# Optimization experiments

Hardware: AMD Instinct MI355X
Metric: run time of the kernel (lower is better)

The kernel has to match this reference:

```python
import jax, jax.numpy as jnp
import numpy as np

S, D = 16384, 1024


def setup_inputs() -> dict:
    key = jax.random.key(0)
    ks = jax.random.split(key, 7)
    stdv = 1.0 / np.sqrt(D)
    u = lambda k, shape: jax.random.uniform(k, shape, jnp.float32, -stdv, stdv)
    return {
        "x": jax.random.normal(ks[0], (S, D), jnp.float32),
        "Wq": u(ks[1], (D, D)), "bq": u(ks[2], (D,)),
        "Wk": u(ks[3], (D, D)), "bk": u(ks[4], (D,)),
        "Wv": u(ks[5], (D, D)), "bv": u(ks[6], (D,)),
    }


def reference(x, Wq, bq, Wk, bk, Wv, bv):
    # torch.nn.Linear: y = x @ W^T + b
    q = x @ Wq.T + bq          # [S, D]
    k = x @ Wk.T + bk          # [S, D]
    v = x @ Wv.T + bv          # [S, D]
    d = x.shape[-1]
    # NOTE: faithful to source -- scores are over the FEATURE axis: [D, D]
    scores = jnp.einsum('sd,se->de', q, k) / jnp.sqrt(jnp.float32(d))
    attn = jax.nn.softmax(scores, axis=-1)   # [D, D]
    out = v @ attn                           # [S, D]
    return out, attn
```

## Files before the change

kernel.cpp:

```cpp
#include <hip/hip_runtime.h>
#include <hip/hip_bf16.h>
#include <stdint.h>


#define S_ 16384
#define D_ 1024

typedef _Float16 half8 __attribute__((ext_vector_type(8)));
typedef _Float16 half4 __attribute__((ext_vector_type(4)));
typedef float f32x4 __attribute__((ext_vector_type(4)));

__device__ __forceinline__ void gload_lds16(const _Float16* g, _Float16* l) {
    __builtin_amdgcn_global_load_lds(
        (const __attribute__((address_space(1))) void*)g,
        (__attribute__((address_space(3))) void*)l, 16, 0, 0);
}

#define VM8() do { asm volatile("s_waitcnt vmcnt(8)" ::: "memory"); __builtin_amdgcn_sched_barrier(0); } while (0)
#define VM0() do { asm volatile("s_waitcnt vmcnt(0)" ::: "memory"); __builtin_amdgcn_sched_barrier(0); } while (0)
#define BAR() __builtin_amdgcn_s_barrier()
#define LGKM0() do { asm volatile("s_waitcnt lgkmcnt(0)" ::: "memory"); __builtin_amdgcn_sched_barrier(0); } while (0)
#define LGKM8() do { asm volatile("s_waitcnt lgkmcnt(8)" ::: "memory"); __builtin_amdgcn_sched_barrier(0); } while (0)
#define PRIO1() __builtin_amdgcn_s_setprio(1)
#define PRIO0() __builtin_amdgcn_s_setprio(0)

#define STAGEA(H, KT, NX) do { \
    const _Float16* _s = srcA + (size_t)((H) * 128) * lda + (size_t)(KT) * 64; \
    _Float16* _d = AsS + (NX) * 16384 + ((H) * 128 + 8 * w) * 64; \
    gload_lds16(_s, _d); \
    gload_lds16(_s + (size_t)64 * lda, _d + 4096); \
} while (0)

#define STAGEB(H, KT, NX) do { \
    const _Float16* _s = srcB + (size_t)((H) * 128) * ldb + (size_t)(KT) * 64; \
    _Float16* _d = BsS + (NX) * 16384 + ((H) * 128 + 8 * w) * 64; \
    gload_lds16(_s, _d); \
    gload_lds16(_s + (size_t)64 * ldb, _d + 4096); \
} while (0)

#define READA(PA, QA) do { _Pragma("unroll") \
    for (int fm = 0; fm < 4; ++fm) { \
        af[fm][0] = *(const half8*)((PA) + (((QA) * 128 + fm * 16) << 7) + cx0); \
        af[fm][1] = *(const half8*)((PA) + (((QA) * 128 + fm * 16) << 7) + cx1); } \
} while (0)

#define READB(PB, BF, QB) do { _Pragma("unroll") \
    for (int fn = 0; fn < 2; ++fn) { \
        BF[fn][0] = *(const half8*)((PB) + (((QB) * 128 + fn * 16) << 7) + cx0); \
        BF[fn][1] = *(const half8*)((PB) + (((QB) * 128 + fn * 16) << 7) + cx1); } \
} while (0)

#define MFMAB(QA, QB, BF) do { _Pragma("unroll") \
    for (int fm = 0; fm < 4; ++fm) { _Pragma("unroll") \
        for (int fn = 0; fn < 2; ++fn) { \
            f32x4 _c = acc[(QA) * 4 + fm][(QB) * 2 + fn]; \
            _c = __builtin_amdgcn_mfma_f32_16x16x32_f16(af[fm][0], BF[fn][0], _c, 0, 0, 0); \
            _c = __builtin_amdgcn_mfma_f32_16x16x32_f16(af[fm][1], BF[fn][1], _c, 0, 0, 0); \
            acc[(QA) * 4 + fm][(QB) * 2 + fn] = _c; } } \
} while (0)

template <int F16OUT, int BIAS>
__global__ __launch_bounds__(512, 2)
void gemm256(const _Float16* __restrict__ A, const _Float16* __restrict__ B,
             void* __restrict__ C, const float* __restrict__ bias,
             int lda, int ldb, int ldc, int ksub, long long mn,
             int ntx, int ntxy, int cpx) {
    __shared__ _Float16 As[2][16384];
    __shared__ _Float16 Bs[2][16384];
    const int t = threadIdx.x;
    const int l = t & 63;
    const int w = t >> 6;
    const int wm = w >> 2, wn = w & 3;

    const int hb = blockIdx.x;
    const int lg = (hb & 7) * cpx + (hb >> 3);
    const int bz = lg / ntxy;
    const int rem = lg - bz * ntxy;
    const int by = rem / ntx;
    const int bx = rem - by * ntx;
    const size_t m0 = (size_t)by * 256;
    const size_t n0 = (size_t)bx * 256;
    const size_t k0 = (size_t)bz * (size_t)ksub;
    const long long coff = (long long)bz * mn;

    const int colsw = 8 * ((l & 7) ^ (l >> 3));
    const _Float16* srcA = A + (m0 + 8 * w + (l >> 3)) * (size_t)lda + k0 + colsw;
    const _Float16* srcB = B + (n0 + 8 * w + (l >> 3)) * (size_t)ldb + k0 + colsw;
    _Float16* AsS = &As[0][0];
    _Float16* BsS = &Bs[0][0];

    const int cx0 = (((l >> 4) << 4)) ^ ((l & 7) << 4);
    const int cx1 = (64 + ((l >> 4) << 4)) ^ ((l & 7) << 4);
    const char* basePA = (const char*)AsS + ((wm * 64 + (l & 15)) << 7);
    const char* basePB = (const char*)BsS + ((wn * 32 + (l & 15)) << 7);

    f32x4 acc[8][4] = {};
    half8 af[4][2], bf0[2][2], bf1[2][2];

    const int nk = ksub >> 6;

    STAGEA(0, 0, 0); STAGEB(0, 0, 0); STAGEB(1, 0, 0); STAGEA(1, 0, 0);
    STAGEA(0, 1, 1); STAGEB(0, 1, 1); STAGEB(1, 1, 1); STAGEA(1, 1, 1);

    for (int kt = 0; kt < nk; ++kt) {
        const int p = kt & 1;
        const int ks = kt + 2;
        const bool hs = ks < nk;
        const char* pA = basePA + p * 32768;
        const char* pB = basePB + p * 32768;

        if (kt == nk - 1) VM0(); else VM8();
        BAR();

        READA(pA, 0); READB(pB, bf0, 0);
        LGKM8();
        BAR(); LGKM0();
        PRIO1(); MFMAB(0, 0, bf0); PRIO0(); BAR();

        READB(pB, bf1, 1);
        if (hs) { STAGEA(0, ks, p); STAGEB(0, ks, p); }
        BAR(); LGKM0();
        PRIO1(); MFMAB(0, 1, bf1); PRIO0(); BAR();

        READA(pA, 1);
        if (hs) STAGEB(1, ks, p);
        BAR(); LGKM0();
        PRIO1(); MFMAB(1, 1, bf1); PRIO0(); BAR();

        if (hs) STAGEA(1, ks, p);
        PRIO1(); MFMAB(1, 0, bf0); PRIO0(); BAR();
    }

    char* lmy = (char*)AsS + w * 16384;
    const int cr = (l >> 4) << 2;
    const int cc = l & 15;

    if (F16OUT) {
        _Float16* lw = (_Float16*)lmy;
#pragma unroll
        for (int h = 0; h < 2; ++h) {
#pragma unroll
            for (int mm = 0; mm < 4; ++mm) {
#pragma unroll
                for (int n = 0; n < 4; ++n) {
                    const int lcol = (n >> 1) * 32 + (n & 1) * 16 + cc;
                    const int lrow = mm * 16 + cr;
#pragma unroll
                    for (int r = 0; r < 4; ++r)
                        lw[(lrow + r) * 68 + lcol] = (_Float16)acc[4 * h + mm][n][r];
                }
            }
            LGKM0();
            const size_t grow0 = m0 + (size_t)h * 128 + wm * 64;
#pragma unroll
            for (int i = 0; i < 32; ++i) {
                const int lrow = i * 2 + (l >> 5);
                const int lcol2 = (l & 31) * 2;
                const uint32_t v = *(const uint32_t*)(lw + lrow * 68 + lcol2);
                const int qb = lcol2 >> 5;
                const size_t col = n0 + qb * 128 + wn * 32 + (lcol2 & 31);
                *(uint32_t*)((_Float16*)C + coff + (long long)(grow0 + lrow) * ldc + col) = v;
            }
            LGKM0();
        }
    } else {
        float* lw = (float*)lmy;
        float bb4[4];
#pragma unroll
        for (int n = 0; n < 4; ++n) {
            const size_t col = n0 + (n >> 1) * 128 + wn * 32 + (n & 1) * 16 + cc;
            bb4[n] = BIAS ? bias[col] : 0.f;
        }
#pragma unroll
        for (int h = 0; h < 4; ++h) {
#pragma unroll
            for (int mm = 0; mm < 2; ++mm) {
#pragma unroll
                for (int n = 0; n < 4; ++n) {
                    const int lcol = (n >> 1) * 32 + (n & 1) * 16 + cc;
                    const int lrow = mm * 16 + cr;
#pragma unroll
                    for (int r = 0; r < 4; ++r)
                        lw[(lrow + r) * 68 + lcol] = acc[2 * h + mm][n][r] + bb4[n];
                }
            }
            LGKM0();
            const size_t grow0 = m0 + (size_t)(h >> 1) * 128 + wm * 64 + (h & 1) * 32;
#pragma unroll
            for (int i = 0; i < 8; ++i) {
                const int lrow = i * 4 + (l >> 4);
                const int lcol = (l & 15) * 4;
                const f32x4 v = *(const f32x4*)(lw + lrow * 68 + lcol);
                const int qb = lcol >> 5;
                const size_t col = n0 + qb * 128 + wn * 32 + (lcol & 31);
                *(f32x4*)((float*)C + coff + (long long)(grow0 + lrow) * ldc + col) = v;
            }
            LGKM0();
        }
    }
}

__global__ __launch_bounds__(256, 2)
void gemm_abt(const _Float16* __restrict__ A, const _Float16* __restrict__ B,
              float* __restrict__ C, const float* __restrict__ bias,
              int bias_mode, int lda, int ldb, int ldc, int ksub,
              float scale, long long mn) {
    const int t = threadIdx.x;
    const int lane = t & 63;
    const int wave = t >> 6;
    const int wr = (wave >> 1) * 64;
    const int wc = (wave & 1) * 64;
    const size_t m0 = (size_t)blockIdx.y * 128;
    const size_t n0 = (size_t)blockIdx.x * 128;
    const size_t k0 = (size_t)blockIdx.z * (size_t)ksub;
    const long long coff = (long long)blockIdx.z * mn;

    __shared__ _Float16 As[128 * 32];
    __shared__ _Float16 Bs[128 * 32];

    f32x4 acc[4][4] = {};

    const _Float16* a0 = A + (m0 + (size_t)(t >> 2)) * (size_t)lda + k0 + (t & 3) * 8;
    const _Float16* a1 = a0 + (size_t)64 * lda;
    const _Float16* b0 = B + (n0 + (size_t)(t >> 2)) * (size_t)ldb + k0 + (t & 3) * 8;
    const _Float16* b1 = b0 + (size_t)64 * ldb;
    _Float16* AsW0 = As + wave * 512;
    _Float16* AsW1 = As + 2048 + wave * 512;
    _Float16* BsW0 = Bs + wave * 512;
    _Float16* BsW1 = Bs + 2048 + wave * 512;

    const int nk = ksub >> 5;
    for (int kt = 0; kt < nk; ++kt) {
        __syncthreads();
        gload_lds16(a0, AsW0);
        gload_lds16(a1, AsW1);
        gload_lds16(b0, BsW0);
        gload_lds16(b1, BsW1);
        a0 += 32; a1 += 32; b0 += 32; b1 += 32;
        __syncthreads();

        half8 af[4], bf[4];
#pragma unroll
        for (int i = 0; i < 4; ++i)
            af[i] = *(const half8*)(As + (wr + i * 16 + (lane & 15)) * 32 + (lane >> 4) * 8);
#pragma unroll
        for (int i = 0; i < 4; ++i)
            bf[i] = *(const half8*)(Bs + (wc + i * 16 + (lane & 15)) * 32 + (lane >> 4) * 8);
#pragma unroll
        for (int i = 0; i < 4; ++i)
#pragma unroll
            for (int j = 0; j < 4; ++j)
                acc[i][j] = __builtin_amdgcn_mfma_f32_16x16x32_f16(af[i], bf[j], acc[i][j], 0, 0, 0);
    }

    const int cr = (lane >> 4) * 4;
    const int cc = lane & 15;
#pragma unroll
    for (int i = 0; i < 4; ++i) {
#pragma unroll
        for (int j = 0; j < 4; ++j) {
            const size_t row0 = m0 + wr + i * 16 + cr;
            const size_t col = n0 + wc + j * 16 + cc;
            const float bcol = (bias_mode == 2) ? bias[col] : 0.f;
#pragma unroll
            for (int r = 0; r < 4; ++r) {
                float val = acc[i][j][r] * scale + bcol;
                C[coff + (long long)(row0 + r) * ldc + col] = val;
            }
        }
    }
}

__global__ void cast2_f32_f16(const float* __restrict__ inA, _Float16* __restrict__ outA,
                              const float* __restrict__ inB, _Float16* __restrict__ outB,
                              int n8) {
    int i = blockIdx.x * 256 + threadIdx.x;
    const float* in = inA;
    _Float16* out = outA;
    if (i >= n8) { i -= n8; in = inB; out = outB; }
    const f32x4* p = (const f32x4*)in + (size_t)i * 2;
    f32x4 x0 = p[0], x1 = p[1];
    half8 h;
    h[0] = (_Float16)x0[0]; h[1] = (_Float16)x0[1];
    h[2] = (_Float16)x0[2]; h[3] = (_Float16)x0[3];
    h[4] = (_Float16)x1[0]; h[5] = (_Float16)x1[1];
    h[6] = (_Float16)x1[2]; h[7] = (_Float16)x1[3];
    ((half8*)out)[i] = h;
}

template <int WRITE_ROW, int COLSUM>
__global__ __launch_bounds__(256)
void cast_transpose(const float* __restrict__ in, _Float16* __restrict__ outRow,
                    _Float16* __restrict__ outT, float* __restrict__ msum, int ldT) {
    __shared__ _Float16 tile[64][66];
    __shared__ float red[16][16][4];
    const int t = threadIdx.x;
    const int c0 = blockIdx.x * 64;
    const int r0 = blockIdx.y * 64;
    const int cg = t & 15;
    const int rb = t >> 4;
    f32x4 csum = {};
#pragma unroll
    for (int it = 0; it < 4; ++it) {
        const int rr = rb + it * 16;
        f32x4 v = *(const f32x4*)(in + (size_t)(r0 + rr) * 1024 + c0 + cg * 4);
        if (COLSUM) { csum[0] += v[0]; csum[1] += v[1]; csum[2] += v[2]; csum[3] += v[3]; }
        _Float16 h0 = (_Float16)v[0], h1 = (_Float16)v[1];
        _Float16 h2 = (_Float16)v[2], h3 = (_Float16)v[3];
        tile[rr][cg * 4 + 0] = h0; tile[rr][cg * 4 + 1] = h1;
        tile[rr][cg * 4 + 2] = h2; tile[rr][cg * 4 + 3] = h3;
        if (WRITE_ROW) {
            half4 h = {h0, h1, h2, h3};
            *(half4*)(outRow + (size_t)(r0 + rr) * 1024 + c0 + cg * 4) = h;
        }
    }
    if (COLSUM) {
        red[rb][cg][0] = csum[0]; red[rb][cg][1] = csum[1];
        red[rb][cg][2] = csum[2]; red[rb][cg][3] = csum[3];
    }
    __syncthreads();
    if (COLSUM && t < 64) {
        float s = 0.f;
#pragma unroll
        for (int k = 0; k < 16; ++k) s += red[k][t >> 2][t & 3];
        atomicAdd(msum + c0 + t, s);
    }
    const int i = t >> 2, ch = (t & 3) * 16;
    half8 h0v, h1v;
#pragma unroll
    for (int j = 0; j < 8; ++j) h0v[j] = tile[ch + j][i];
#pragma unroll
    for (int j = 0; j < 8; ++j) h1v[j] = tile[ch + 8 + j][i];
    *(half8*)(outT + (size_t)(c0 + i) * ldT + r0 + ch) = h0v;
    *(half8*)(outT + (size_t)(c0 + i) * ldT + r0 + ch + 8) = h1v;
}

__global__ void zero_vec(float* __restrict__ p, int n) {
    int i = blockIdx.x * 256 + threadIdx.x;
    if (i < n) p[i] = 0.f;
}

__global__ __launch_bounds__(256)
void u2w_kernel(const float* __restrict__ Wq, const float* __restrict__ Wk,
                const float* __restrict__ bq, const float* __restrict__ m,
                float* __restrict__ u2, float* __restrict__ w) {
    const int bid = blockIdx.x;
    const int t = threadIdx.x;
    const float* W = (bid < 1024) ? Wq : Wk;
    const int row = (bid < 1024) ? bid : bid - 1024;
    float s = 0.f;
#pragma unroll
    for (int it = 0; it < 4; ++it) {
        const int i = t + it * 256;
        s += W[(size_t)row * 1024 + i] * m[i];
    }
    for (int o = 32; o; o >>= 1) s += __shfl_xor(s, o);
    __shared__ float red[4];
    if ((t & 63) == 0) red[t >> 6] = s;
    __syncthreads();
    if (t == 0) {
        float tot = red[0] + red[1] + red[2] + red[3];
        if (bid < 1024) u2[bid] = tot + 16384.0f * bq[bid];
        else w[row] = tot;
    }
}

__global__ __launch_bounds__(256)
void reduce_g(const _Float16* __restrict__ part, _Float16* __restrict__ G16) {
    const size_t off = ((size_t)blockIdx.x * 256 + threadIdx.x) * 8;
    float s[8] = {};
    for (int z = 0; z < 16; ++z) {
        half8 v = *(const half8*)(part + (size_t)z * 1048576 + off);
#pragma unroll
        for (int j = 0; j < 8; ++j) s[j] += (float)v[j];
    }
    half8 o;
#pragma unroll
    for (int j = 0; j < 8; ++j) o[j] = (_Float16)s[j];
    *(half8*)(G16 + off) = o;
}

__global__ __launch_bounds__(256)
void reduce_cast(const float* __restrict__ part, _Float16* __restrict__ outh,
                 int nz, float scale) {
    const int idx = (blockIdx.x * 256 + threadIdx.x) * 4;
    f32x4 s = {};
    for (int z = 0; z < nz; ++z) {
        f32x4 v = *(const f32x4*)(part + (size_t)z * 1048576 + idx);
        s[0] += v[0]; s[1] += v[1]; s[2] += v[2]; s[3] += v[3];
    }
    half4 h;
    h[0] = (_Float16)(s[0] * scale); h[1] = (_Float16)(s[1] * scale);
    h[2] = (_Float16)(s[2] * scale); h[3] = (_Float16)(s[3] * scale);
    *(half4*)(outh + idx) = h;
}

__global__ __launch_bounds__(256)
void softmax_rows(const float* __restrict__ part, const float* __restrict__ u2,
                  const float* __restrict__ bq, const float* __restrict__ bk,
                  const float* __restrict__ w,
                  float* __restrict__ P, _Float16* __restrict__ PT) {
    const int a = blockIdx.x;
    const int t = threadIdx.x;
    __shared__ float red[8];
    const size_t off = (size_t)a * 1024 + t * 4;
    f32x4 s = {};
#pragma unroll
    for (int z = 0; z < 4; ++z) {
        f32x4 v = *(const f32x4*)(part + (size_t)z * 1048576 + off);
        s[0] += v[0]; s[1] += v[1]; s[2] += v[2]; s[3] += v[3];
    }
    const float ru = u2[a], rb = bq[a];
    f32x4 bk4 = *(const f32x4*)(bk + t * 4);
    f32x4 w4 = *(const f32x4*)(w + t * 4);
#pragma unroll
    for (int j = 0; j < 4; ++j) s[j] = (s[j] + ru * bk4[j] + rb * w4[j]) * 0.03125f;

    float m = fmaxf(fmaxf(s[0], s[1]), fmaxf(s[2], s[3]));
    for (int o = 32; o; o >>= 1) m = fmaxf(m, __shfl_xor(m, o));
    if ((t & 63) == 0) red[t >> 6] = m;
    __syncthreads();
    m = fmaxf(fmaxf(red[0], red[1]), fmaxf(red[2], red[3]));

    float e0 = expf(s[0] - m), e1 = expf(s[1] - m);
    float e2 = expf(s[2] - m), e3 = expf(s[3] - m);
    float sum = e0 + e1 + e2 + e3;
    for (int o = 32; o; o >>= 1) sum += __shfl_xor(sum, o);
    if ((t & 63) == 0) red[4 + (t >> 6)] = sum;
    __syncthreads();
    sum = red[4] + red[5] + red[6] + red[7];
    const float inv = 1.0f / sum;

    f32x4 o4 = {e0 * inv, e1 * inv, e2 * inv, e3 * inv};
    *(f32x4*)(P + off) = o4;
    const int b = t * 4;
    PT[(size_t)(b + 0) * 1024 + a] = (_Float16)o4[0];
    PT[(size_t)(b + 1) * 1024 + a] = (_Float16)o4[1];
    PT[(size_t)(b + 2) * 1024 + a] = (_Float16)o4[2];
    PT[(size_t)(b + 3) * 1024 + a] = (_Float16)o4[3];
}

__global__ __launch_bounds__(256)
void attn_bv(const float* __restrict__ attn, const float* __restrict__ bv,
             float* __restrict__ c) {
    const int j = blockIdx.x * 256 + threadIdx.x;
    const int a0 = blockIdx.y * 64;
    float s = 0.f;
#pragma unroll 4
    for (int k = 0; k < 64; ++k) {
        const int a = a0 + k;
        s += attn[(size_t)a * 1024 + j] * bv[a];
    }
    atomicAdd(c + j, s);
}

extern "C" void kernel_launch(void* const* d_in, const int* in_sizes, int n_in,
                              void* d_out, int out_size, void* d_ws, size_t ws_size,
                              hipStream_t stream) {
    const float* x  = (const float*)d_in[0];
    const float* Wq = (const float*)d_in[1];
    const float* bq = (const float*)d_in[2];
    const float* Wk = (const float*)d_in[3];
    const float* bk = (const float*)d_in[4];
    const float* Wv = (const float*)d_in[5];
    const float* bv = (const float*)d_in[6];
    float* out  = (float*)d_out;
    float* attn = out + (size_t)S_ * D_;

    char* ws = (char*)d_ws;
    float*    part  = (float*)ws;
    _Float16* partH = (_Float16*)ws;
    _Float16* x16   = (_Float16*)(ws + 33554432);
    _Float16* xT16  = (_Float16*)(ws + 67108864);
    _Float16* wq16  = (_Float16*)(ws + 100663296);
    _Float16* wk16  = (_Float16*)(ws + 102760448);
    _Float16* wvT16 = (_Float16*)(ws + 104857600);
    _Float16* G16   = (_Float16*)(ws + 106954752);
    _Float16* U16   = (_Float16*)(ws + 109051904);
    _Float16* PT    = (_Float16*)(ws + 111149056);
    _Float16* MT16  = (_Float16*)(ws + 113246208);
    float*    mvec  = (float*)(ws + 115343360);
    float*    u2    = mvec + 1024;
    float*    wv    = u2 + 1024;
    float*    cvec  = wv + 1024;

    zero_vec<<<16, 256, 0, stream>>>(mvec, 4096);
    cast_transpose<1, 1><<<dim3(16, 256), 256, 0, stream>>>(x, x16, xT16, mvec, S_);
    cast2_f32_f16<<<1024, 256, 0, stream>>>(Wq, wq16, Wk, wk16, D_ * D_ / 8);
    cast_transpose<0, 0><<<dim3(16, 16), 256, 0, stream>>>(Wv, nullptr, wvT16, nullptr, D_);
    u2w_kernel<<<2048, 256, 0, stream>>>(Wq, Wk, bq, mvec, u2, wv);

    gemm256<1, 0><<<256, 512, 0, stream>>>(xT16, xT16, (void*)partH, nullptr,
                                           16384, 16384, 1024, 1024, 1048576LL,
                                           4, 16, 32);
    reduce_g<<<512, 256, 0, stream>>>(partH, G16);
    gemm_abt<<<dim3(8, 8, 4), 256, 0, stream>>>(wq16, G16, part, nullptr, 0,
                                                1024, 1024, 1024, 256, 1.0f, 1048576);
    reduce_cast<<<1024, 256, 0, stream>>>(part, U16, 4, 1.0f);
    gemm_abt<<<dim3(8, 8, 4), 256, 0, stream>>>(U16, wk16, part, nullptr, 0,
                                                1024, 1024, 1024, 256, 1.0f, 1048576);
    softmax_rows<<<1024, 256, 0, stream>>>(part, u2, bq, bk, wv, attn, PT);
    attn_bv<<<dim3(4, 16), 256, 0, stream>>>(attn, bv, cvec);
    gemm_abt<<<dim3(8, 8, 4), 256, 0, stream>>>(PT, wvT16, part, nullptr, 0,
                                                1024, 1024, 1024, 256, 1.0f, 1048576);
    reduce_cast<<<1024, 256, 0, stream>>>(part, MT16, 4, 1.0f);
    gemm256<0, 1><<<256, 512, 0, stream>>>(x16, MT16, (void*)out, cvec,
                                           1024, 1024, 1024, 1024, 0LL,
                                           4, 256, 32);
}
```

Measured before the change: 192.4 us.

## Drop split-K for small GEMMs, fuse epilogues, merge weight prep kernels

The three 1024^3 GEMMs no longer use 4-way split-K with separate reduce kernels. Each now runs the full K loop on an 8x8 grid and writes fp16 or the bias-corrected, scaled scores directly, so softmax only reads scores. The weight cast, Wv transpose and u2/w dot products are merged into one prep kernel, and the big GEMM epilogue stores become nontemporal. This removes launches and partial-sum memory traffic, but each small GEMM now runs only 64 blocks, which leaves most CUs idle.

```diff
diff --git a/kernel.cpp b/kernel.cpp
--- a/kernel.cpp
+++ b/kernel.cpp
@@ -159,7 +159,8 @@
                 const uint32_t v = *(const uint32_t*)(lw + lrow * 68 + lcol2);
                 const int qb = lcol2 >> 5;
                 const size_t col = n0 + qb * 128 + wn * 32 + (lcol2 & 31);
-                *(uint32_t*)((_Float16*)C + coff + (long long)(grow0 + lrow) * ldc + col) = v;
+                __builtin_nontemporal_store(v,
+                    (uint32_t*)((_Float16*)C + coff + (long long)(grow0 + lrow) * ldc + col));
             }
             LGKM0();
         }
@@ -193,18 +194,21 @@
                 const f32x4 v = *(const f32x4*)(lw + lrow * 68 + lcol);
                 const int qb = lcol >> 5;
                 const size_t col = n0 + qb * 128 + wn * 32 + (lcol & 31);
-                *(f32x4*)((float*)C + coff + (long long)(grow0 + lrow) * ldc + col) = v;
+                __builtin_nontemporal_store(v,
+                    (f32x4*)((float*)C + coff + (long long)(grow0 + lrow) * ldc + col));
             }
             LGKM0();
         }
     }
 }
 
+template <int MODE>
 __global__ __launch_bounds__(256, 2)
-void gemm_abt(const _Float16* __restrict__ A, const _Float16* __restrict__ B,
-              float* __restrict__ C, const float* __restrict__ bias,
-              int bias_mode, int lda, int ldb, int ldc, int ksub,
-              float scale, long long mn) {
+void gemm_s(const _Float16* __restrict__ A, const _Float16* __restrict__ B,
+            void* __restrict__ C,
+            const float* __restrict__ u2v, const float* __restrict__ bqv,
+            const float* __restrict__ bkv, const float* __restrict__ wvv,
+            int lda, int ldb, int ldc) {
     const int t = threadIdx.x;
     const int lane = t & 63;
     const int wave = t >> 6;
@@ -212,25 +216,22 @@
     const int wc = (wave & 1) * 64;
     const size_t m0 = (size_t)blockIdx.y * 128;
     const size_t n0 = (size_t)blockIdx.x * 128;
-    const size_t k0 = (size_t)blockIdx.z * (size_t)ksub;
-    const long long coff = (long long)blockIdx.z * mn;
 
     __shared__ _Float16 As[128 * 32];
     __shared__ _Float16 Bs[128 * 32];
 
     f32x4 acc[4][4] = {};
 
-    const _Float16* a0 = A + (m0 + (size_t)(t >> 2)) * (size_t)lda + k0 + (t & 3) * 8;
+    const _Float16* a0 = A + (m0 + (size_t)(t >> 2)) * (size_t)lda + (t & 3) * 8;
     const _Float16* a1 = a0 + (size_t)64 * lda;
-    const _Float16* b0 = B + (n0 + (size_t)(t >> 2)) * (size_t)ldb + k0 + (t & 3) * 8;
+    const _Float16* b0 = B + (n0 + (size_t)(t >> 2)) * (size_t)ldb + (t & 3) * 8;
     const _Float16* b1 = b0 + (size_t)64 * ldb;
     _Float16* AsW0 = As + wave * 512;
     _Float16* AsW1 = As + 2048 + wave * 512;
     _Float16* BsW0 = Bs + wave * 512;
     _Float16* BsW1 = Bs + 2048 + wave * 512;
 
-    const int nk = ksub >> 5;
-    for (int kt = 0; kt < nk; ++kt) {
+    for (int kt = 0; kt < 32; ++kt) {
         __syncthreads();
         gload_lds16(a0, AsW0);
         gload_lds16(a1, AsW1);
@@ -261,31 +262,18 @@
         for (int j = 0; j < 4; ++j) {
             const size_t row0 = m0 + wr + i * 16 + cr;
             const size_t col = n0 + wc + j * 16 + cc;
-            const float bcol = (bias_mode == 2) ? bias[col] : 0.f;
 #pragma unroll
             for (int r = 0; r < 4; ++r) {
-                float val = acc[i][j][r] * scale + bcol;
-                C[coff + (long long)(row0 + r) * ldc + col] = val;
+                if (MODE == 1) {
+                    ((_Float16*)C)[(row0 + r) * (size_t)ldc + col] = (_Float16)acc[i][j][r];
+                } else {
+                    const float val = (acc[i][j][r] + u2v[row0 + r] * bkv[col]
+                                       + bqv[row0 + r] * wvv[col]) * 0.03125f;
+                    ((float*)C)[(row0 + r) * (size_t)ldc + col] = val;
+                }
             }
         }
     }
-}
-
-__global__ void cast2_f32_f16(const float* __restrict__ inA, _Float16* __restrict__ outA,
-                              const float* __restrict__ inB, _Float16* __restrict__ outB,
-                              int n8) {
-    int i = blockIdx.x * 256 + threadIdx.x;
-    const float* in = inA;
-    _Float16* out = outA;
-    if (i >= n8) { i -= n8; in = inB; out = outB; }
-    const f32x4* p = (const f32x4*)in + (size_t)i * 2;
-    f32x4 x0 = p[0], x1 = p[1];
-    half8 h;
-    h[0] = (_Float16)x0[0]; h[1] = (_Float16)x0[1];
-    h[2] = (_Float16)x0[2]; h[3] = (_Float16)x0[3];
-    h[4] = (_Float16)x1[0]; h[5] = (_Float16)x1[1];
-    h[6] = (_Float16)x1[2]; h[7] = (_Float16)x1[3];
-    ((half8*)out)[i] = h;
 }
 
 template <int WRITE_ROW, int COLSUM>
@@ -335,34 +323,83 @@
     *(half8*)(outT + (size_t)(c0 + i) * ldT + r0 + ch + 8) = h1v;
 }
 
+__global__ __launch_bounds__(256)
+void prep_w(const float* __restrict__ Wq, const float* __restrict__ Wk,
+            const float* __restrict__ Wv, const float* __restrict__ bq,
+            const float* __restrict__ m,
+            _Float16* __restrict__ wq16, _Float16* __restrict__ wk16,
+            _Float16* __restrict__ wvT16,
+            float* __restrict__ u2, float* __restrict__ w) {
+    __shared__ _Float16 tile[64][66];
+    __shared__ float wred[4];
+    const int b = blockIdx.x;
+    const int t = threadIdx.x;
+
+    if (b < 1024) {
+        const bool isQ = b < 512;
+        const int bb = isQ ? b : b - 512;
+        const float* W = isQ ? Wq : Wk;
+        _Float16* o = isQ ? wq16 : wk16;
+        const size_t base = (size_t)bb * 2048 + (size_t)t * 8;
+        const f32x4* p = (const f32x4*)(W + base);
+        f32x4 x0 = p[0], x1 = p[1];
+        half8 h;
+        h[0] = (_Float16)x0[0]; h[1] = (_Float16)x0[1];
+        h[2] = (_Float16)x0[2]; h[3] = (_Float16)x0[3];
+        h[4] = (_Float16)x1[0]; h[5] = (_Float16)x1[1];
+        h[6] = (_Float16)x1[2]; h[7] = (_Float16)x1[3];
+        ((half8*)o)[bb * 256 + t] = h;
+        const int col = (t * 8) & 1023;
+        f32x4 m0 = *(const f32x4*)(m + col);
+        f32x4 m1 = *(const f32x4*)(m + col + 4);
+        float s = x0[0] * m0[0] + x0[1] * m0[1] + x0[2] * m0[2] + x0[3] * m0[3]
+                + x1[0] * m1[0] + x1[1] * m1[1] + x1[2] * m1[2] + x1[3] * m1[3];
+        for (int o2 = 32; o2; o2 >>= 1) s += __shfl_xor(s, o2);
+        if ((t & 63) == 0) wred[t >> 6] = s;
+        __syncthreads();
+        if (t == 0) {
+            const int rA = 2 * bb, rB = 2 * bb + 1;
+            const float vA = wred[0] + wred[1];
+            const float vB = wred[2] + wred[3];
+            if (isQ) {
+                u2[rA] = vA + 16384.0f * bq[rA];
+                u2[rB] = vB + 16384.0f * bq[rB];
+            } else {
+                w[rA] = vA;
+                w[rB] = vB;
+            }
+        }
+        return;
+    }
+
+    const int bb = b - 1024;
+    const int c0 = (bb & 15) * 64;
+    const int r0 = (bb >> 4) * 64;
+    const int cg = t & 15;
+    const int rb = t >> 4;
+#pragma unroll
+    for (int it = 0; it < 4; ++it) {
+        const int rr = rb + it * 16;
+        f32x4 v = *(const f32x4*)(Wv + (size_t)(r0 + rr) * 1024 + c0 + cg * 4);
+        tile[rr][cg * 4 + 0] = (_Float16)v[0];
+        tile[rr][cg * 4 + 1] = (_Float16)v[1];
+        tile[rr][cg * 4 + 2] = (_Float16)v[2];
+        tile[rr][cg * 4 + 3] = (_Float16)v[3];
+    }
+    __syncthreads();
+    const int i = t >> 2, ch = (t & 3) * 16;
+    half8 h0v, h1v;
+#pragma unroll
+    for (int j = 0; j < 8; ++j) h0v[j] = tile[ch + j][i];
+#pragma unroll
+    for (int j = 0; j < 8; ++j) h1v[j] = tile[ch + 8 + j][i];
+    *(half8*)(wvT16 + (size_t)(c0 + i) * 1024 + r0 + ch) = h0v;
+    *(half8*)(wvT16 + (size_t)(c0 + i) * 1024 + r0 + ch + 8) = h1v;
+}
+
 __global__ void zero_vec(float* __restrict__ p, int n) {
     int i = blockIdx.x * 256 + threadIdx.x;
     if (i < n) p[i] = 0.f;
-}
-
-__global__ __launch_bounds__(256)
-void u2w_kernel(const float* __restrict__ Wq, const float* __restrict__ Wk,
-                const float* __restrict__ bq, const float* __restrict__ m,
-                float* __restrict__ u2, float* __restrict__ w) {
-    const int bid = blockIdx.x;
-    const int t = threadIdx.x;
-    const float* W = (bid < 1024) ? Wq : Wk;
-    const int row = (bid < 1024) ? bid : bid - 1024;
-    float s = 0.f;
-#pragma unroll
-    for (int it = 0; it < 4; ++it) {
-        const int i = t + it * 256;
-        s += W[(size_t)row * 1024 + i] * m[i];
-    }
-    for (int o = 32; o; o >>= 1) s += __shfl_xor(s, o);
-    __shared__ float red[4];
-    if ((t & 63) == 0) red[t >> 6] = s;
-    __syncthreads();
-    if (t == 0) {
-        float tot = red[0] + red[1] + red[2] + red[3];
-        if (bid < 1024) u2[bid] = tot + 16384.0f * bq[bid];
-        else w[row] = tot;
-    }
 }
 
 __global__ __launch_bounds__(256)
@@ -381,40 +418,13 @@
 }
 
 __global__ __launch_bounds__(256)
-void reduce_cast(const float* __restrict__ part, _Float16* __restrict__ outh,
-                 int nz, float scale) {
-    const int idx = (blockIdx.x * 256 + threadIdx.x) * 4;
-    f32x4 s = {};
-    for (int z = 0; z < nz; ++z) {
-        f32x4 v = *(const f32x4*)(part + (size_t)z * 1048576 + idx);
-        s[0] += v[0]; s[1] += v[1]; s[2] += v[2]; s[3] += v[3];
-    }
-    half4 h;
-    h[0] = (_Float16)(s[0] * scale); h[1] = (_Float16)(s[1] * scale);
-    h[2] = (_Float16)(s[2] * scale); h[3] = (_Float16)(s[3] * scale);
-    *(half4*)(outh + idx) = h;
-}
-
-__global__ __launch_bounds__(256)
-void softmax_rows(const float* __restrict__ part, const float* __restrict__ u2,
-                  const float* __restrict__ bq, const float* __restrict__ bk,
-                  const float* __restrict__ w,
+void softmax_rows(const float* __restrict__ scores,
                   float* __restrict__ P, _Float16* __restrict__ PT) {
     const int a = blockIdx.x;
     const int t = threadIdx.x;
     __shared__ float red[8];
     const size_t off = (size_t)a * 1024 + t * 4;
-    f32x4 s = {};
-#pragma unroll
-    for (int z = 0; z < 4; ++z) {
-        f32x4 v = *(const f32x4*)(part + (size_t)z * 1048576 + off);
-        s[0] += v[0]; s[1] += v[1]; s[2] += v[2]; s[3] += v[3];
-    }
-    const float ru = u2[a], rb = bq[a];
-    f32x4 bk4 = *(const f32x4*)(bk + t * 4);
-    f32x4 w4 = *(const f32x4*)(w + t * 4);
-#pragma unroll
-    for (int j = 0; j < 4; ++j) s[j] = (s[j] + ru * bk4[j] + rb * w4[j]) * 0.03125f;
+    f32x4 s = *(const f32x4*)(scores + off);
 
     float m = fmaxf(fmaxf(s[0], s[1]), fmaxf(s[2], s[3]));
     for (int o = 32; o; o >>= 1) m = fmaxf(m, __shfl_xor(m, o));
@@ -468,7 +478,7 @@
     float* attn = out + (size_t)S_ * D_;
 
     char* ws = (char*)d_ws;
-    float*    part  = (float*)ws;
+    float*    scores = (float*)ws;
     _Float16* partH = (_Float16*)ws;
     _Float16* x16   = (_Float16*)(ws + 33554432);
     _Float16* xT16  = (_Float16*)(ws + 67108864);
@@ -486,24 +496,24 @@
 
     zero_vec<<<16, 256, 0, stream>>>(mvec, 4096);
     cast_transpose<1, 1><<<dim3(16, 256), 256, 0, stream>>>(x, x16, xT16, mvec, S_);
-    cast2_f32_f16<<<1024, 256, 0, stream>>>(Wq, wq16, Wk, wk16, D_ * D_ / 8);
-    cast_transpose<0, 0><<<dim3(16, 16), 256, 0, stream>>>(Wv, nullptr, wvT16, nullptr, D_);
-    u2w_kernel<<<2048, 256, 0, stream>>>(Wq, Wk, bq, mvec, u2, wv);
+    prep_w<<<1280, 256, 0, stream>>>(Wq, Wk, Wv, bq, mvec,
+                                     wq16, wk16, wvT16, u2, wv);
 
     gemm256<1, 0><<<256, 512, 0, stream>>>(xT16, xT16, (void*)partH, nullptr,
                                            16384, 16384, 1024, 1024, 1048576LL,
                                            4, 16, 32);
     reduce_g<<<512, 256, 0, stream>>>(partH, G16);
-    gemm_abt<<<dim3(8, 8, 4), 256, 0, stream>>>(wq16, G16, part, nullptr, 0,
-                                                1024, 1024, 1024, 256, 1.0f, 1048576);
-    reduce_cast<<<1024, 256, 0, stream>>>(part, U16, 4, 1.0f);
-    gemm_abt<<<dim3(8, 8, 4), 256, 0, stream>>>(U16, wk16, part, nullptr, 0,
-                                                1024, 1024, 1024, 256, 1.0f, 1048576);
-    softmax_rows<<<1024, 256, 0, stream>>>(part, u2, bq, bk, wv, attn, PT);
+    gemm_s<1><<<dim3(8, 8), 256, 0, stream>>>(wq16, G16, (void*)U16,
+                                              nullptr, nullptr, nullptr, nullptr,
+                                              1024, 1024, 1024);
+    gemm_s<2><<<dim3(8, 8), 256, 0, stream>>>(U16, wk16, (void*)scores,
+                                              u2, bq, bk, wv,
+                                              1024, 1024, 1024);
+    softmax_rows<<<1024, 256, 0, stream>>>(scores, attn, PT);
     attn_bv<<<dim3(4, 16), 256, 0, stream>>>(attn, bv, cvec);
-    gemm_abt<<<dim3(8, 8, 4), 256, 0, stream>>>(PT, wvT16, part, nullptr, 0,
-                                                1024, 1024, 1024, 256, 1.0f, 1048576);
-    reduce_cast<<<1024, 256, 0, stream>>>(part, MT16, 4, 1.0f);
+    gemm_s<1><<<dim3(8, 8), 256, 0, stream>>>(PT, wvT16, (void*)MT16,
+                                              nullptr, nullptr, nullptr, nullptr,
+                                              1024, 1024, 1024);
     gemm256<0, 1><<<256, 512, 0, stream>>>(x16, MT16, (void*)out, cvec,
                                            1024, 1024, 1024, 1024, 0LL,
                                            4, 256, 32);
```

After: 197.3 us. 1.03x slower.
